# Kernel optimization log

Hardware: AMD Instinct MI355X
Metric: run time of the kernel (lower is better)

## Reference

```python
import jax, jax.numpy as jnp
import numpy as np

B, T, E, H, V = 128, 400, 128, 128, 50000
H2, H4, H6 = 2 * H, 4 * H, 6 * H


def setup_inputs() -> dict:
    key = jax.random.key(0)
    ks = jax.random.split(key, 16)
    s = 0.05
    return dict(
        input_ids=jax.random.randint(ks[0], (B, 1), 0, V),
        pre_hidden=jax.random.normal(ks[1], (1, B, H2), jnp.float32),
        pre_cell=jax.random.normal(ks[2], (1, B, H2), jnp.float32),
        enc_outputs=jax.random.normal(ks[3], (B, T, H2), jnp.float32),
        source_input=jax.random.randint(ks[4], (B, T), 0, V),
        coverage=jax.random.uniform(ks[5], (B, 1, T), jnp.float32),
        emb_table=s * jax.random.normal(ks[6], (V, E), jnp.float32),
        w_ih=s * jax.random.normal(ks[7], (4 * H2, E), jnp.float32),
        w_hh=s * jax.random.normal(ks[8], (4 * H2, H2), jnp.float32),
        b_ih=jnp.zeros((4 * H2,), jnp.float32),
        b_hh=jnp.zeros((4 * H2,), jnp.float32),
        w_align=s * jax.random.normal(ks[9], (1, H6), jnp.float32),
        b_align=jnp.zeros((1,), jnp.float32),
        w_cov=s * jax.random.normal(ks[10], (H2, 1), jnp.float32),
        b_cov=jnp.zeros((H2,), jnp.float32),
        w_fc1=s * jax.random.normal(ks[11], (H4, H4), jnp.float32),
        b_fc1=jnp.zeros((H4,), jnp.float32),
        w_fc2=s * jax.random.normal(ks[12], (V, H4), jnp.float32),
        b_fc2=jnp.zeros((V,), jnp.float32),
        w_gen=s * jax.random.normal(ks[13], (1, H4 + E), jnp.float32),
        b_gen=jnp.zeros((1,), jnp.float32),
    )


def reference(input_ids, pre_hidden, pre_cell, enc_outputs, source_input, coverage,
              emb_table, w_ih, w_hh, b_ih, b_hh, w_align, b_align, w_cov, b_cov,
              w_fc1, b_fc1, w_fc2, b_fc2, w_gen, b_gen):
    # embedding lookup (flag=False path: no dropout)
    emb = emb_table[input_ids[:, 0]]                      # [B,E]
    # single-step LSTM (PyTorch gate order i,f,g,o; hidden size 2H)
    h0, c0 = pre_hidden[0], pre_cell[0]                   # [B,2H]
    gates = emb @ w_ih.T + b_ih + h0 @ w_hh.T + b_hh      # [B,8H]
    i, f, g, o = jnp.split(gates, 4, axis=-1)
    c = jax.nn.sigmoid(f) * c0 + jax.nn.sigmoid(i) * jnp.tanh(g)
    h = jax.nn.sigmoid(o) * jnp.tanh(c)                   # [B,2H]
    # coverage feature + attention over encoder steps
    cov_feat = coverage.transpose(0, 2, 1) @ w_cov.T + b_cov        # [B,T,2H]
    h_rep = jnp.broadcast_to(h[:, None, :], enc_outputs.shape)     # [B,T,2H]
    combine = jnp.concatenate([enc_outputs, h_rep, cov_feat], -1)  # [B,T,6H]
    scores = jnp.tanh(combine @ w_align.T + b_align)               # [B,T,1]
    attn = jax.nn.softmax(scores, axis=1)                          # [B,T,1]
    attn_bt = attn[:, :, 0]                                        # [B,T]
    cov_bt = coverage[:, 0, :]
    cov_loss = jnp.sum(jnp.minimum(attn_bt, cov_bt))
    new_cov = coverage + attn_bt[:, None, :]                       # [B,1,T]
    # context + vocab distribution
    context = jnp.einsum('bt,bte->be', attn_bt, enc_outputs)       # [B,2H]
    fc = jnp.tanh(jnp.concatenate([h, context], -1) @ w_fc1.T + b_fc1)
    pvocab = jax.nn.softmax(fc @ w_fc2.T + b_fc2, axis=1)          # [B,V]
    # copy distribution: fused batched scatter-add (replaces per-batch one-hot matmul loop)
    b_idx = jnp.arange(attn_bt.shape[0])[:, None]
    copy = jnp.zeros_like(pvocab).at[b_idx, source_input].add(attn_bt)
    # generation probability and mixture
    gen_in = jnp.concatenate([context, h, emb], -1)                # [B,4H+E]
    pgen = jax.nn.sigmoid(gen_in @ w_gen.T + b_gen)                # [B,1]
    out = pvocab * pgen + copy * (1.0 - pgen)
    return (out, h[None], c[None], attn_bt[:, None, :], copy, new_cov, cov_loss)
```

## Files before the change

### kernel.cpp

```cpp
#include <hip/hip_runtime.h>
#include <hip/hip_bf16.h>
#include <math.h>

#define B_  128
#define T_  400
#define E_  128
#define H2_ 256
#define H4_ 512
#define V_  50000
#define G4_ 1024
#define KACT 384

#define OFF_H       6400000
#define OFF_C       6432768
#define OFF_ATTN    6465536
#define OFF_COPY    6516736
#define OFF_NEWCOV 12916736
#define OFF_COVLOSS 12967936

#define WS_ACT   0
#define WS_GATES (WS_ACT + KACT*B_)
#define WS_HC    (WS_GATES + G4_*B_)
#define WS_FCB   (WS_HC + H4_*B_)
#define WS_SC    (WS_FCB + H4_*B_/2)
#define WS_ATTN  (WS_SC + B_*T_)
#define WS_CTXP  (WS_ATTN + B_*T_)
#define WS_SMP   (WS_CTXP + B_*8*H2_)
#define WS_HDOT  (WS_SMP + B_*8*2)
#define WS_COVP  (WS_HDOT + B_)
#define WS_PGEN  (WS_COVP + B_)
#define WS_MAX   (WS_PGEN + B_)
#define WS_INV   (WS_MAX + B_)
#define WS_AB    (WS_INV + B_)

typedef __attribute__((ext_vector_type(8))) short bf16x8;
typedef __attribute__((ext_vector_type(4))) float f32x4;
typedef __attribute__((ext_vector_type(16))) float f32x16;

__device__ inline float sigmoidf_(float x){ return 1.f/(1.f+__expf(-x)); }

__device__ inline short f2bf(float x){
  __hip_bfloat16 h = __float2bfloat16(x);
  return *reinterpret_cast<short*>(&h);
}

__device__ inline float blk_reduce_sum(float v, float* red){
  int t = threadIdx.x;
  red[t] = v; __syncthreads();
  for (int s = 128; s > 0; s >>= 1){ if (t < s) red[t] += red[t+s]; __syncthreads(); }
  float r = red[0]; __syncthreads(); return r;
}
__device__ inline float blk_reduce_max(float v, float* red){
  int t = threadIdx.x;
  red[t] = v; __syncthreads();
  for (int s = 128; s > 0; s >>= 1){ if (t < s) red[t] = fmaxf(red[t], red[t+s]); __syncthreads(); }
  float r = red[0]; __syncthreads(); return r;
}

__global__ __launch_bounds__(256) void k_zero(float* __restrict__ p){
  size_t i = ((size_t)blockIdx.x*256 + threadIdx.x)*4;
  if (i < (size_t)B_*V_)
    *(float4*)&p[i] = make_float4(0.f,0.f,0.f,0.f);
}

__global__ __launch_bounds__(256) void k_act(const int* __restrict__ ids,
    const float* __restrict__ pre_h, const float* __restrict__ emb_table,
    const float* __restrict__ w_align, const float* __restrict__ w_cov,
    const float* __restrict__ b_cov, float* __restrict__ act,
    float* __restrict__ ab){
  __shared__ float red[256];
  int t = threadIdx.x;
  int idx = blockIdx.x*256 + t;
  int k = idx >> 7, b = idx & 127;
  float v = (k < E_) ? emb_table[(size_t)ids[b]*E_ + k]
                     : pre_h[b*H2_ + (k - E_)];
  act[idx] = v;
  if (blockIdx.x == 0) {
    float wa = w_align[2*H2_ + t];
    float alpha = blk_reduce_sum(w_cov[t]*wa, red);
    float beta  = blk_reduce_sum(b_cov[t]*wa, red);
    if (t == 0) { ab[0] = alpha; ab[1] = beta; }
  }
}

__global__ __launch_bounds__(256) void k_gates(const float* __restrict__ act,
    const float* __restrict__ w_ih, const float* __restrict__ w_hh,
    const float* __restrict__ b_ih, const float* __restrict__ b_hh,
    float* __restrict__ gates){
  __shared__ float wt[8][KACT];
  int t = threadIdx.x; int j0 = blockIdx.x*8;
  for (int idx = t; idx < 8*KACT; idx += 256) {
    int r = idx / KACT, k = idx % KACT;
    int j = j0 + r;
    wt[r][k] = (k < E_) ? w_ih[j*E_ + k] : w_hh[j*H2_ + (k - E_)];
  }
  __syncthreads();
  int jq = t >> 7, b = t & 127;
  float acc[4] = {0.f,0.f,0.f,0.f};
  for (int k = 0; k < KACT; ++k) {
    float a = act[k*B_ + b];
    #pragma unroll
    for (int jj = 0; jj < 4; ++jj) acc[jj] += wt[jq*4+jj][k]*a;
  }
  #pragma unroll
  for (int jj = 0; jj < 4; ++jj) {
    int j = j0 + jq*4 + jj;
    gates[j*B_ + b] = acc[jj] + b_ih[j] + b_hh[j];
  }
}

__global__ __launch_bounds__(256) void k_lstm(const float* __restrict__ gates,
    const float* __restrict__ pre_c, const float* __restrict__ w_align,
    float* __restrict__ o_h, float* __restrict__ o_c,
    float* __restrict__ hc, float* __restrict__ hdot){
  __shared__ float red[256];
  int b = blockIdx.x, k = threadIdx.x;
  float i_ = gates[(0*H2_ + k)*B_ + b];
  float f_ = gates[(1*H2_ + k)*B_ + b];
  float g_ = gates[(2*H2_ + k)*B_ + b];
  float o_ = gates[(3*H2_ + k)*B_ + b];
  float c = sigmoidf_(f_)*pre_c[b*H2_ + k] + sigmoidf_(i_)*tanhf(g_);
  float h = sigmoidf_(o_)*tanhf(c);
  o_h[b*H2_ + k] = h;
  o_c[b*H2_ + k] = c;
  hc[k*B_ + b] = h;
  float s = blk_reduce_sum(h * w_align[H2_ + k], red);
  if (k == 0) hdot[b] = s;
}

__global__ __launch_bounds__(256) void k_scores(const float* __restrict__ enc,
    const float* __restrict__ cov, const float* __restrict__ w_align,
    const float* __restrict__ b_align, const float* __restrict__ hdot,
    const float* __restrict__ ab, float* __restrict__ sc){
  int b = blockIdx.y, c = blockIdx.x;
  int t = threadIdx.x, wave = t >> 6, lane = t & 63;
  float4 wa4 = *(const float4*)&w_align[lane*4];
  float hd = hdot[b], alpha = ab[0], beta = ab[1], ba = b_align[0];
  int t0 = c*50;
  for (int tt = t0 + wave; tt < t0 + 50; tt += 4) {
    const float4* ep = (const float4*)&enc[((size_t)b*T_ + tt)*H2_];
    float4 e4 = ep[lane];
    float d = e4.x*wa4.x + e4.y*wa4.y + e4.z*wa4.z + e4.w*wa4.w;
    #pragma unroll
    for (int m = 32; m >= 1; m >>= 1) d += __shfl_xor(d, m);
    if (lane == 0)
      sc[b*T_ + tt] = tanhf(d + hd + alpha*cov[b*T_ + tt] + beta + ba);
  }
}

__global__ __launch_bounds__(256) void k_soft(const float* __restrict__ sc_in,
    const float* __restrict__ cov, const int* __restrict__ src,
    float* __restrict__ o_attn, float* __restrict__ o_newcov,
    float* __restrict__ o_copy, float* __restrict__ covp,
    float* __restrict__ attn_ws){
  __shared__ float red[256];
  int b = blockIdx.x, t = threadIdx.x;
  float x1 = sc_in[b*T_ + t];
  float x2 = (t + 256 < T_) ? sc_in[b*T_ + t + 256] : -1e30f;
  float mx = blk_reduce_max(fmaxf(x1, x2), red);
  float e1 = __expf(x1 - mx);
  float e2 = (t + 256 < T_) ? __expf(x2 - mx) : 0.f;
  float sum = blk_reduce_sum(e1 + e2, red);
  float inv = 1.f/sum;
  float cl;
  {
    float a1 = e1*inv; float c1 = cov[b*T_ + t];
    attn_ws[b*T_ + t] = a1;
    o_attn[b*T_ + t] = a1;
    o_newcov[b*T_ + t] = c1 + a1;
    atomicAdd(&o_copy[(size_t)b*V_ + src[b*T_ + t]], a1);
    cl = fminf(a1, c1);
  }
  if (t + 256 < T_) {
    float a2 = e2*inv; float c2 = cov[b*T_ + t + 256];
    attn_ws[b*T_ + t + 256] = a2;
    o_attn[b*T_ + t + 256] = a2;
    o_newcov[b*T_ + t + 256] = c2 + a2;
    atomicAdd(&o_copy[(size_t)b*V_ + src[b*T_ + t + 256]], a2);
    cl += fminf(a2, c2);
  }
  float clsum = blk_reduce_sum(cl, red);
  if (t == 0) covp[b] = clsum;
}

__global__ __launch_bounds__(256) void k_ctx(const float* __restrict__ enc,
    const float* __restrict__ attn_ws, float* __restrict__ ctxp){
  __shared__ float a_s[50];
  int b = blockIdx.y, c = blockIdx.x, e = threadIdx.x;
  int t0 = c*50;
  if (e < 50) a_s[e] = attn_ws[b*T_ + t0 + e];
  __syncthreads();
  float acc = 0.f;
  #pragma unroll 5
  for (int i = 0; i < 50; ++i)
    acc += a_s[i] * enc[((size_t)b*T_ + t0 + i)*H2_ + e];
  ctxp[((size_t)b*8 + c)*H2_ + e] = acc;
}

__global__ __launch_bounds__(256) void k_ctxpgen(const float* __restrict__ ctxp,
    const int* __restrict__ ids, const float* __restrict__ emb_table,
    const float* __restrict__ w_gen, const float* __restrict__ b_gen,
    float* __restrict__ hc, float* __restrict__ pgen){
  __shared__ float red[256];
  int b = blockIdx.x, t = threadIdx.x;
  float ctx = 0.f;
  #pragma unroll
  for (int c = 0; c < 8; ++c) ctx += ctxp[((size_t)b*8 + c)*H2_ + t];
  hc[(H2_ + t)*B_ + b] = ctx;
  float p = ctx*w_gen[t] + hc[t*B_ + b]*w_gen[H2_ + t];
  if (t < E_) p += emb_table[(size_t)ids[b]*E_ + t]*w_gen[2*H2_ + t];
  float s = blk_reduce_sum(p, red);
  if (t == 0) pgen[b] = sigmoidf_(s + b_gen[0]);
}

__global__ __launch_bounds__(256) void k_fc1(const float* __restrict__ hc,
    const float* __restrict__ w_fc1, const float* __restrict__ b_fc1,
    short* __restrict__ fcb){
  __shared__ float wt[16][H4_];
  int t = threadIdx.x; int j0 = blockIdx.x*16;
  for (int idx = t; idx < 16*H4_; idx += 256) {
    int r = idx >> 9, k = idx & 511;
    wt[r][k] = w_fc1[(j0 + r)*H4_ + k];
  }
  __syncthreads();
  int jq = t >> 7, b = t & 127;
  float acc[8] = {};
  for (int k = 0; k < H4_; ++k) {
    float a = hc[k*B_ + b];
    #pragma unroll
    for (int jj = 0; jj < 8; ++jj) acc[jj] += wt[jq*8+jj][k]*a;
  }
  bf16x8 pack;
  #pragma unroll
  for (int jj = 0; jj < 8; ++jj) {
    int j = j0 + jq*8 + jj;
    pack[jj] = f2bf(tanhf(acc[jj] + b_fc1[j]));
  }
  *(bf16x8*)&fcb[(size_t)b*H4_ + j0 + jq*8] = pack;
}

__global__ __launch_bounds__(256, 2) void k_gemm2m(const short* __restrict__ fcb,
    const float* __restrict__ w_fc2, const float* __restrict__ b_fc2,
    float* __restrict__ logits){
  __shared__ __attribute__((aligned(16))) char lds[49152];
  int t = threadIdx.x;
  int w = t >> 6, l = t & 63;
  int ln = l & 31, g2 = l >> 5;
  int v0 = blockIdx.x*128;
  int v = v0 + w*32 + ln;
  int vl = w*32 + ln;

  int ar0 = t >> 2,         as0 = t & 3;
  int ar1 = (256 + t) >> 2, as1 = (256 + t) & 3;
  int aoff0 = as0*2048 + ((ar0 ^ (as0 << 1)) & 127)*16;
  int aoff1 = as1*2048 + ((ar1 ^ (as1 << 1)) & 127)*16;
  const short* ag0 = fcb + ar0*H4_ + as0*8;
  const short* ag1 = fcb + ar1*H4_ + as1*8;
  int woffs[4]; const float* wgs[4];
  #pragma unroll
  for (int p = 0; p < 4; ++p) {
    int i = p*256 + t;
    int row = i >> 3, kg = i & 7;
    woffs[p] = 8192 + kg*2048 + ((row ^ kg) & 127)*16;
    int vr = v0 + row; if (vr >= V_) vr = V_ - 1;
    wgs[p] = w_fc2 + (size_t)vr*H4_ + kg*4;
  }

  f32x16 acc0 = {}, acc1 = {}, acc2 = {}, acc3 = {};

  bf16x8 aE0, aE1; f32x4 wE0, wE1, wE2, wE3;
  bf16x8 aO0, aO1; f32x4 wO0, wO1, wO2, wO3;

  #define LOADSET(A0, A1, W0, W1, W2, W3, c) {                                \
    A0 = *(const bf16x8*)(ag0 + (c)*32);                                      \
    A1 = *(const bf16x8*)(ag1 + (c)*32);                                      \
    W0 = *(const f32x4*)(wgs[0] + (c)*32);                                    \
    W1 = *(const f32x4*)(wgs[1] + (c)*32);                                    \
    W2 = *(const f32x4*)(wgs[2] + (c)*32);                                    \
    W3 = *(const f32x4*)(wgs[3] + (c)*32);                                    \
  }
  #define WRITESET(A0, A1, W0, W1, W2, W3, bi) {                              \
    char* bb = lds + (bi)*24576;                                              \
    *(bf16x8*)(bb + aoff0) = A0;                                              \
    *(bf16x8*)(bb + aoff1) = A1;                                              \
    *(f32x4*)(bb + woffs[0]) = W0;                                            \
    *(f32x4*)(bb + woffs[1]) = W1;                                            \
    *(f32x4*)(bb + woffs[2]) = W2;                                            \
    *(f32x4*)(bb + woffs[3]) = W3;                                            \
  }

  LOADSET(aE0, aE1, wE0, wE1, wE2, wE3, 0)
  LOADSET(aO0, aO1, wO0, wO1, wO2, wO3, 1)
  WRITESET(aE0, aE1, wE0, wE1, wE2, wE3, 0)
  LOADSET(aE0, aE1, wE0, wE1, wE2, wE3, 2)
  __syncthreads();

  for (int c = 0; c < 16; ++c) {
    if (c + 1 < 16) {
      if ((c + 1) & 1) {
        WRITESET(aO0, aO1, wO0, wO1, wO2, wO3, 1)
        if (c + 3 < 16) LOADSET(aO0, aO1, wO0, wO1, wO2, wO3, c + 3)
      } else {
        WRITESET(aE0, aE1, wE0, wE1, wE2, wE3, 0)
        if (c + 3 < 16) LOADSET(aE0, aE1, wE0, wE1, wE2, wE3, c + 3)
      }
    }
    char* Ab = lds + (c & 1)*24576;
    char* Wb = Ab + 8192;
    #pragma unroll
    for (int s = 0; s < 2; ++s) {
      int sg = s*2 + g2;
      bf16x8 a0 = *(const bf16x8*)(Ab + sg*2048 + (((0*32+ln) ^ (sg<<1)) & 127)*16);
      bf16x8 a1 = *(const bf16x8*)(Ab + sg*2048 + (((1*32+ln) ^ (sg<<1)) & 127)*16);
      bf16x8 a2 = *(const bf16x8*)(Ab + sg*2048 + (((2*32+ln) ^ (sg<<1)) & 127)*16);
      bf16x8 a3 = *(const bf16x8*)(Ab + sg*2048 + (((3*32+ln) ^ (sg<<1)) & 127)*16);
      int kgA = s*4 + g2*2;
      f32x4 f0 = *(const f32x4*)(Wb + kgA*2048 + ((vl ^ kgA) & 127)*16);
      int kgB = kgA + 1;
      f32x4 f1 = *(const f32x4*)(Wb + kgB*2048 + ((vl ^ kgB) & 127)*16);
      bf16x8 bf;
      bf[0]=f2bf(f0[0]); bf[1]=f2bf(f0[1]); bf[2]=f2bf(f0[2]); bf[3]=f2bf(f0[3]);
      bf[4]=f2bf(f1[0]); bf[5]=f2bf(f1[1]); bf[6]=f2bf(f1[2]); bf[7]=f2bf(f1[3]);
      acc0 = __builtin_amdgcn_mfma_f32_32x32x16_bf16(a0, bf, acc0, 0, 0, 0);
      acc1 = __builtin_amdgcn_mfma_f32_32x32x16_bf16(a1, bf, acc1, 0, 0, 0);
      acc2 = __builtin_amdgcn_mfma_f32_32x32x16_bf16(a2, bf, acc2, 0, 0, 0);
      acc3 = __builtin_amdgcn_mfma_f32_32x32x16_bf16(a3, bf, acc3, 0, 0, 0);
    }
    __syncthreads();
  }
  #undef LOADSET
  #undef WRITESET

  if (v < V_) {
    float bias = b_fc2[v];
    #pragma unroll
    for (int r = 0; r < 16; ++r) {
      int brow = (r & 3) + 8*(r >> 2) + 4*g2;
      logits[(size_t)(brow)*V_ + v]      = acc0[r] + bias;
      logits[(size_t)(32 + brow)*V_ + v] = acc1[r] + bias;
      logits[(size_t)(64 + brow)*V_ + v] = acc2[r] + bias;
      logits[(size_t)(96 + brow)*V_ + v] = acc3[r] + bias;
    }
  }
}

__global__ __launch_bounds__(256) void k_smp(const float* __restrict__ logits,
    float* __restrict__ smp){
  __shared__ float rm[256], rs[256];
  int b = blockIdx.y, c = blockIdx.x, t = threadIdx.x;
  int v0 = c*6250, v1 = v0 + 6250;
  float m = -1e30f, s = 0.f;
  for (int v = v0 + t; v < v1; v += 256) {
    float x = logits[(size_t)b*V_ + v];
    float nm = fmaxf(m, x);
    s = s*__expf(m - nm) + __expf(x - nm);
    m = nm;
  }
  rm[t] = m; rs[t] = s; __syncthreads();
  for (int k = 128; k > 0; k >>= 1) {
    if (t < k) {
      float m1 = rm[t], s1 = rs[t], m2 = rm[t+k], s2 = rs[t+k];
      float nm = fmaxf(m1, m2);
      rm[t] = nm; rs[t] = s1*__expf(m1-nm) + s2*__expf(m2-nm);
    }
    __syncthreads();
  }
  if (t == 0) { smp[(b*8+c)*2] = rm[0]; smp[(b*8+c)*2+1] = rs[0]; }
}

__global__ __launch_bounds__(128) void k_smred_cl(const float* __restrict__ smp,
    const float* __restrict__ covp, float* __restrict__ mx,
    float* __restrict__ inv, float* __restrict__ o_cl){
  __shared__ float red[128];
  int t = threadIdx.x;
  float m = -1e30f, s = 0.f;
  #pragma unroll
  for (int c = 0; c < 8; ++c) {
    float m2 = smp[(t*8+c)*2], s2 = smp[(t*8+c)*2+1];
    float nm = fmaxf(m, m2);
    s = s*__expf(m - nm) + s2*__expf(m2 - nm);
    m = nm;
  }
  mx[t] = m; inv[t] = 1.f/s;
  red[t] = covp[t]; __syncthreads();
  for (int k = 64; k > 0; k >>= 1){ if (t < k) red[t] += red[t+k]; __syncthreads(); }
  if (t == 0) o_cl[0] = red[0];
}

__global__ __launch_bounds__(256) void k_final(const float* __restrict__ copy,
    const float* __restrict__ mx, const float* __restrict__ inv_s,
    const float* __restrict__ pgen, float* __restrict__ out){
  size_t gid = (size_t)blockIdx.x*256 + threadIdx.x;
  int b = (int)(gid / (V_/4));
  int v = (int)(gid % (V_/4))*4;
  size_t idx = (size_t)b*V_ + v;
  float m = mx[b], is = inv_s[b], pg = pgen[b];
  float4 lg = *(const float4*)&out[idx];
  float4 cp = *(const float4*)&copy[idx];
  float4 o;
  o.x = __expf(lg.x - m)*is*pg + cp.x*(1.f - pg);
  o.y = __expf(lg.y - m)*is*pg + cp.y*(1.f - pg);
  o.z = __expf(lg.z - m)*is*pg + cp.z*(1.f - pg);
  o.w = __expf(lg.w - m)*is*pg + cp.w*(1.f - pg);
  *(float4*)&out[idx] = o;
}

extern "C" void kernel_launch(void* const* d_in, const int* in_sizes, int n_in,
                              void* d_out, int out_size, void* d_ws, size_t ws_size,
                              hipStream_t stream) {
  const int*   ids       = (const int*)  d_in[0];
  const float* pre_h     = (const float*)d_in[1];
  const float* pre_c     = (const float*)d_in[2];
  const float* enc       = (const float*)d_in[3];
  const int*   src       = (const int*)  d_in[4];
  const float* cov       = (const float*)d_in[5];
  const float* emb_table = (const float*)d_in[6];
  const float* w_ih      = (const float*)d_in[7];
  const float* w_hh      = (const float*)d_in[8];
  const float* b_ih      = (const float*)d_in[9];
  const float* b_hh      = (const float*)d_in[10];
  const float* w_align   = (const float*)d_in[11];
  const float* b_align   = (const float*)d_in[12];
  const float* w_cov     = (const float*)d_in[13];
  const float* b_cov     = (const float*)d_in[14];
  const float* w_fc1     = (const float*)d_in[15];
  const float* b_fc1     = (const float*)d_in[16];
  const float* w_fc2     = (const float*)d_in[17];
  const float* b_fc2     = (const float*)d_in[18];
  const float* w_gen     = (const float*)d_in[19];
  const float* b_gen     = (const float*)d_in[20];

  float* out = (float*)d_out;
  float* ws  = (float*)d_ws;

  float* o_out    = out;
  float* o_h      = out + OFF_H;
  float* o_c      = out + OFF_C;
  float* o_attn   = out + OFF_ATTN;
  float* o_copy   = out + OFF_COPY;
  float* o_newcov = out + OFF_NEWCOV;
  float* o_cl     = out + OFF_COVLOSS;

  k_zero <<<(B_*V_/4 + 255)/256, 256, 0, stream>>>(o_copy);
  k_act  <<<192, 256, 0, stream>>>(ids, pre_h, emb_table, w_align, w_cov, b_cov,
                                   ws + WS_ACT, ws + WS_AB);
  k_gates<<<128, 256, 0, stream>>>(ws + WS_ACT, w_ih, w_hh, b_ih, b_hh, ws + WS_GATES);
  k_lstm <<<128, 256, 0, stream>>>(ws + WS_GATES, pre_c, w_align, o_h, o_c,
                                   ws + WS_HC, ws + WS_HDOT);
  k_scores<<<dim3(8,128), 256, 0, stream>>>(enc, cov, w_align, b_align,
                                   ws + WS_HDOT, ws + WS_AB, ws + WS_SC);
  k_soft <<<128, 256, 0, stream>>>(ws + WS_SC, cov, src, o_attn, o_newcov, o_copy,
                                   ws + WS_COVP, ws + WS_ATTN);
  k_ctx  <<<dim3(8,128), 256, 0, stream>>>(enc, ws + WS_ATTN, ws + WS_CTXP);
  k_ctxpgen<<<128, 256, 0, stream>>>(ws + WS_CTXP, ids, emb_table, w_gen, b_gen,
                                   ws + WS_HC, ws + WS_PGEN);
  k_fc1  <<<32, 256, 0, stream>>>(ws + WS_HC, w_fc1, b_fc1, (short*)(ws + WS_FCB));
  k_gemm2m<<<(V_ + 127)/128, 256, 0, stream>>>((const short*)(ws + WS_FCB),
                                   w_fc2, b_fc2, o_out);
  k_smp  <<<dim3(8,128), 256, 0, stream>>>(o_out, ws + WS_SMP);
  k_smred_cl<<<1, 128, 0, stream>>>(ws + WS_SMP, ws + WS_COVP,
                                   ws + WS_MAX, ws + WS_INV, o_cl);
  k_final<<<(int)(((size_t)B_*V_/4)/256), 256, 0, stream>>>(
      o_copy, ws + WS_MAX, ws + WS_INV, ws + WS_PGEN, o_out);
}
```

Baseline: 146.3 us.

## Fuse context computation into score kernel with chunk-local softmax rescaling

The score kernel now keeps each 50-row chunk of encoder outputs in shared memory, computes a chunk-local max and exponentials, and accumulates an unnormalized partial context along with the chunk max. The separate context kernel, which re-read all encoder outputs (about 52 MB), is removed. The pgen kernel rescales the partials using the global max and inverse sum that the softmax kernel now saves. This adds 51 KB of LDS per block, which lowers occupancy. Separately, the fc2 GEMM launch bound is raised to 3 blocks per SM.

```diff
diff --git a/kernel.cpp b/kernel.cpp
--- a/kernel.cpp
+++ b/kernel.cpp
@@ -23,15 +23,17 @@
 #define WS_HC    (WS_GATES + G4_*B_)
 #define WS_FCB   (WS_HC + H4_*B_)
 #define WS_SC    (WS_FCB + H4_*B_/2)
-#define WS_ATTN  (WS_SC + B_*T_)
-#define WS_CTXP  (WS_ATTN + B_*T_)
+#define WS_CTXP  (WS_SC + B_*T_)
 #define WS_SMP   (WS_CTXP + B_*8*H2_)
-#define WS_HDOT  (WS_SMP + B_*8*2)
+#define WS_CHM   (WS_SMP + B_*8*2)
+#define WS_HDOT  (WS_CHM + B_*8)
 #define WS_COVP  (WS_HDOT + B_)
 #define WS_PGEN  (WS_COVP + B_)
 #define WS_MAX   (WS_PGEN + B_)
 #define WS_INV   (WS_MAX + B_)
-#define WS_AB    (WS_INV + B_)
+#define WS_AMX   (WS_INV + B_)
+#define WS_AINV  (WS_AMX + B_)
+#define WS_AB    (WS_AINV + B_)
 
 typedef __attribute__((ext_vector_type(8))) short bf16x8;
 typedef __attribute__((ext_vector_type(4))) float f32x4;
@@ -128,10 +130,14 @@
   if (k == 0) hdot[b] = s;
 }
 
-__global__ __launch_bounds__(256) void k_scores(const float* __restrict__ enc,
+__global__ __launch_bounds__(256) void k_attn2(const float* __restrict__ enc,
     const float* __restrict__ cov, const float* __restrict__ w_align,
     const float* __restrict__ b_align, const float* __restrict__ hdot,
-    const float* __restrict__ ab, float* __restrict__ sc){
+    const float* __restrict__ ab, float* __restrict__ sc,
+    float* __restrict__ ctxp, float* __restrict__ chm){
+  __shared__ float erow[50][H2_];
+  __shared__ float scs[50];
+  __shared__ float red[256];
   int b = blockIdx.y, c = blockIdx.x;
   int t = threadIdx.x, wave = t >> 6, lane = t & 63;
   float4 wa4 = *(const float4*)&w_align[lane*4];
@@ -140,19 +146,32 @@
   for (int tt = t0 + wave; tt < t0 + 50; tt += 4) {
     const float4* ep = (const float4*)&enc[((size_t)b*T_ + tt)*H2_];
     float4 e4 = ep[lane];
+    *(float4*)&erow[tt - t0][lane*4] = e4;
     float d = e4.x*wa4.x + e4.y*wa4.y + e4.z*wa4.z + e4.w*wa4.w;
     #pragma unroll
     for (int m = 32; m >= 1; m >>= 1) d += __shfl_xor(d, m);
-    if (lane == 0)
-      sc[b*T_ + tt] = tanhf(d + hd + alpha*cov[b*T_ + tt] + beta + ba);
-  }
+    if (lane == 0) {
+      float s = tanhf(d + hd + alpha*cov[b*T_ + tt] + beta + ba);
+      scs[tt - t0] = s;
+      sc[b*T_ + tt] = s;
+    }
+  }
+  __syncthreads();
+  float mc = blk_reduce_max(t < 50 ? scs[t] : -1e30f, red);
+  if (t < 50) scs[t] = __expf(scs[t] - mc);
+  __syncthreads();
+  float acc = 0.f;
+  #pragma unroll 5
+  for (int i = 0; i < 50; ++i) acc += scs[i]*erow[i][t];
+  ctxp[((size_t)b*8 + c)*H2_ + t] = acc;
+  if (t == 0) chm[b*8 + c] = mc;
 }
 
 __global__ __launch_bounds__(256) void k_soft(const float* __restrict__ sc_in,
     const float* __restrict__ cov, const int* __restrict__ src,
     float* __restrict__ o_attn, float* __restrict__ o_newcov,
     float* __restrict__ o_copy, float* __restrict__ covp,
-    float* __restrict__ attn_ws){
+    float* __restrict__ amx, float* __restrict__ ainv){
   __shared__ float red[256];
   int b = blockIdx.x, t = threadIdx.x;
   float x1 = sc_in[b*T_ + t];
@@ -162,10 +181,10 @@
   float e2 = (t + 256 < T_) ? __expf(x2 - mx) : 0.f;
   float sum = blk_reduce_sum(e1 + e2, red);
   float inv = 1.f/sum;
+  if (t == 0) { amx[b] = mx; ainv[b] = inv; }
   float cl;
   {
     float a1 = e1*inv; float c1 = cov[b*T_ + t];
-    attn_ws[b*T_ + t] = a1;
     o_attn[b*T_ + t] = a1;
     o_newcov[b*T_ + t] = c1 + a1;
     atomicAdd(&o_copy[(size_t)b*V_ + src[b*T_ + t]], a1);
@@ -173,7 +192,6 @@
   }
   if (t + 256 < T_) {
     float a2 = e2*inv; float c2 = cov[b*T_ + t + 256];
-    attn_ws[b*T_ + t + 256] = a2;
     o_attn[b*T_ + t + 256] = a2;
     o_newcov[b*T_ + t + 256] = c2 + a2;
     atomicAdd(&o_copy[(size_t)b*V_ + src[b*T_ + t + 256]], a2);
@@ -183,29 +201,20 @@
   if (t == 0) covp[b] = clsum;
 }
 
-__global__ __launch_bounds__(256) void k_ctx(const float* __restrict__ enc,
-    const float* __restrict__ attn_ws, float* __restrict__ ctxp){
-  __shared__ float a_s[50];
-  int b = blockIdx.y, c = blockIdx.x, e = threadIdx.x;
-  int t0 = c*50;
-  if (e < 50) a_s[e] = attn_ws[b*T_ + t0 + e];
-  __syncthreads();
-  float acc = 0.f;
-  #pragma unroll 5
-  for (int i = 0; i < 50; ++i)
-    acc += a_s[i] * enc[((size_t)b*T_ + t0 + i)*H2_ + e];
-  ctxp[((size_t)b*8 + c)*H2_ + e] = acc;
-}
-
 __global__ __launch_bounds__(256) void k_ctxpgen(const float* __restrict__ ctxp,
+    const float* __restrict__ chm, const float* __restrict__ amx,
+    const float* __restrict__ ainv,
     const int* __restrict__ ids, const float* __restrict__ emb_table,
     const float* __restrict__ w_gen, const float* __restrict__ b_gen,
     float* __restrict__ hc, float* __restrict__ pgen){
   __shared__ float red[256];
   int b = blockIdx.x, t = threadIdx.x;
+  float M = amx[b], iS = ainv[b];
   float ctx = 0.f;
   #pragma unroll
-  for (int c = 0; c < 8; ++c) ctx += ctxp[((size_t)b*8 + c)*H2_ + t];
+  for (int c = 0; c < 8; ++c)
+    ctx += ctxp[((size_t)b*8 + c)*H2_ + t] * __expf(chm[b*8 + c] - M);
+  ctx *= iS;
   hc[(H2_ + t)*B_ + b] = ctx;
   float p = ctx*w_gen[t] + hc[t*B_ + b]*w_gen[H2_ + t];
   if (t < E_) p += emb_table[(size_t)ids[b]*E_ + t]*w_gen[2*H2_ + t];
@@ -239,7 +248,7 @@
   *(bf16x8*)&fcb[(size_t)b*H4_ + j0 + jq*8] = pack;
 }
 
-__global__ __launch_bounds__(256, 2) void k_gemm2m(const short* __restrict__ fcb,
+__global__ __launch_bounds__(256, 3) void k_gemm2m(const short* __restrict__ fcb,
     const float* __restrict__ w_fc2, const float* __restrict__ b_fc2,
     float* __restrict__ logits){
   __shared__ __attribute__((aligned(16))) char lds[49152];
@@ -447,12 +456,13 @@
   k_gates<<<128, 256, 0, stream>>>(ws + WS_ACT, w_ih, w_hh, b_ih, b_hh, ws + WS_GATES);
   k_lstm <<<128, 256, 0, stream>>>(ws + WS_GATES, pre_c, w_align, o_h, o_c,
                                    ws + WS_HC, ws + WS_HDOT);
-  k_scores<<<dim3(8,128), 256, 0, stream>>>(enc, cov, w_align, b_align,
-                                   ws + WS_HDOT, ws + WS_AB, ws + WS_SC);
+  k_attn2<<<dim3(8,128), 256, 0, stream>>>(enc, cov, w_align, b_align,
+                                   ws + WS_HDOT, ws + WS_AB, ws + WS_SC,
+                                   ws + WS_CTXP, ws + WS_CHM);
   k_soft <<<128, 256, 0, stream>>>(ws + WS_SC, cov, src, o_attn, o_newcov, o_copy,
-                                   ws + WS_COVP, ws + WS_ATTN);
-  k_ctx  <<<dim3(8,128), 256, 0, stream>>>(enc, ws + WS_ATTN, ws + WS_CTXP);
-  k_ctxpgen<<<128, 256, 0, stream>>>(ws + WS_CTXP, ids, emb_table, w_gen, b_gen,
+                                   ws + WS_COVP, ws + WS_AMX, ws + WS_AINV);
+  k_ctxpgen<<<128, 256, 0, stream>>>(ws + WS_CTXP, ws + WS_CHM, ws + WS_AMX,
+                                   ws + WS_AINV, ids, emb_table, w_gen, b_gen,
                                    ws + WS_HC, ws + WS_PGEN);
   k_fc1  <<<32, 256, 0, stream>>>(ws + WS_HC, w_fc1, b_fc1, (short*)(ws + WS_FCB));
   k_gemm2m<<<(V_ + 127)/128, 256, 0, stream>>>((const short*)(ws + WS_FCB),
```

Result: slower. 150.3 us (+2.7%).

## Store logits as bf16 and replace dense copy read with sparse scatter-add

Applied to the files above, without the earlier changes.

The vocab GEMM now writes its logits as bf16 into workspace instead of fp32 into the output buffer, which halves the bytes written by the GEMM and read by the softmax-partial and final kernels. The final mix kernel no longer reads the dense copy tensor. It writes only the scaled softmax term, and a new kernel atomically adds attn*(1-pgen) at the source-token positions. This cuts a full B×V read from the final pass. Rounding logits to bf16 before the exponent adds precision loss in the output probabilities, and the write pattern of the new bf16 stores may be less coalesced.

```diff
diff --git a/kernel.cpp b/kernel.cpp
--- a/kernel.cpp
+++ b/kernel.cpp
@@ -32,6 +32,7 @@
 #define WS_MAX   (WS_PGEN + B_)
 #define WS_INV   (WS_MAX + B_)
 #define WS_AB    (WS_INV + B_)
+#define WS_LOGB  (WS_AB + 16)
 
 typedef __attribute__((ext_vector_type(8))) short bf16x8;
 typedef __attribute__((ext_vector_type(4))) float f32x4;
@@ -42,6 +43,10 @@
 __device__ inline short f2bf(float x){
   __hip_bfloat16 h = __float2bfloat16(x);
   return *reinterpret_cast<short*>(&h);
+}
+__device__ inline float bf2f(unsigned short u){
+  unsigned int x = ((unsigned int)u) << 16;
+  return *reinterpret_cast<float*>(&x);
 }
 
 __device__ inline float blk_reduce_sum(float v, float* red){
@@ -241,7 +246,7 @@
 
 __global__ __launch_bounds__(256, 2) void k_gemm2m(const short* __restrict__ fcb,
     const float* __restrict__ w_fc2, const float* __restrict__ b_fc2,
-    float* __restrict__ logits){
+    short* __restrict__ logb){
   __shared__ __attribute__((aligned(16))) char lds[49152];
   int t = threadIdx.x;
   int w = t >> 6, l = t & 63;
@@ -336,24 +341,27 @@
     #pragma unroll
     for (int r = 0; r < 16; ++r) {
       int brow = (r & 3) + 8*(r >> 2) + 4*g2;
-      logits[(size_t)(brow)*V_ + v]      = acc0[r] + bias;
-      logits[(size_t)(32 + brow)*V_ + v] = acc1[r] + bias;
-      logits[(size_t)(64 + brow)*V_ + v] = acc2[r] + bias;
-      logits[(size_t)(96 + brow)*V_ + v] = acc3[r] + bias;
+      logb[(size_t)(brow)*V_ + v]      = f2bf(acc0[r] + bias);
+      logb[(size_t)(32 + brow)*V_ + v] = f2bf(acc1[r] + bias);
+      logb[(size_t)(64 + brow)*V_ + v] = f2bf(acc2[r] + bias);
+      logb[(size_t)(96 + brow)*V_ + v] = f2bf(acc3[r] + bias);
     }
   }
 }
 
-__global__ __launch_bounds__(256) void k_smp(const float* __restrict__ logits,
+__global__ __launch_bounds__(256) void k_smp(const unsigned short* __restrict__ logb,
     float* __restrict__ smp){
   __shared__ float rm[256], rs[256];
   int b = blockIdx.y, c = blockIdx.x, t = threadIdx.x;
-  int v0 = c*6250, v1 = v0 + 6250;
+  int u0 = c*3125, u1 = u0 + 3125;
+  const unsigned int* lp = (const unsigned int*)(logb + (size_t)b*V_);
   float m = -1e30f, s = 0.f;
-  for (int v = v0 + t; v < v1; v += 256) {
-    float x = logits[(size_t)b*V_ + v];
-    float nm = fmaxf(m, x);
-    s = s*__expf(m - nm) + __expf(x - nm);
+  for (int u = u0 + t; u < u1; u += 256) {
+    unsigned int pr = lp[u];
+    float xa = bf2f((unsigned short)(pr & 0xffff));
+    float xb = bf2f((unsigned short)(pr >> 16));
+    float nm = fmaxf(m, fmaxf(xa, xb));
+    s = s*__expf(m - nm) + __expf(xa - nm) + __expf(xb - nm);
     m = nm;
   }
   rm[t] = m; rs[t] = s; __syncthreads();
@@ -387,22 +395,27 @@
   if (t == 0) o_cl[0] = red[0];
 }
 
-__global__ __launch_bounds__(256) void k_final(const float* __restrict__ copy,
+__global__ __launch_bounds__(256) void k_final(const unsigned short* __restrict__ logb,
     const float* __restrict__ mx, const float* __restrict__ inv_s,
     const float* __restrict__ pgen, float* __restrict__ out){
   size_t gid = (size_t)blockIdx.x*256 + threadIdx.x;
-  int b = (int)(gid / (V_/4));
-  int v = (int)(gid % (V_/4))*4;
-  size_t idx = (size_t)b*V_ + v;
+  int b = (int)(gid / (V_/2));
+  int u = (int)(gid % (V_/2));
   float m = mx[b], is = inv_s[b], pg = pgen[b];
-  float4 lg = *(const float4*)&out[idx];
-  float4 cp = *(const float4*)&copy[idx];
-  float4 o;
-  o.x = __expf(lg.x - m)*is*pg + cp.x*(1.f - pg);
-  o.y = __expf(lg.y - m)*is*pg + cp.y*(1.f - pg);
-  o.z = __expf(lg.z - m)*is*pg + cp.z*(1.f - pg);
-  o.w = __expf(lg.w - m)*is*pg + cp.w*(1.f - pg);
-  *(float4*)&out[idx] = o;
+  unsigned int pr = ((const unsigned int*)(logb + (size_t)b*V_))[u];
+  float2 o;
+  o.x = __expf(bf2f((unsigned short)(pr & 0xffff)) - m)*is*pg;
+  o.y = __expf(bf2f((unsigned short)(pr >> 16)) - m)*is*pg;
+  *(float2*)&out[(size_t)b*V_ + u*2] = o;
+}
+
+__global__ __launch_bounds__(256) void k_scatter(const int* __restrict__ src,
+    const float* __restrict__ attn, const float* __restrict__ pgen,
+    float* __restrict__ out){
+  int b = blockIdx.x, t = threadIdx.x;
+  float c1 = 1.f - pgen[b];
+  for (int tt = t; tt < T_; tt += 256)
+    atomicAdd(&out[(size_t)b*V_ + src[b*T_ + tt]], attn[b*T_ + tt]*c1);
 }
 
 extern "C" void kernel_launch(void* const* d_in, const int* in_sizes, int n_in,
@@ -440,6 +453,7 @@
   float* o_copy   = out + OFF_COPY;
   float* o_newcov = out + OFF_NEWCOV;
   float* o_cl     = out + OFF_COVLOSS;
+  short* logb     = (short*)(ws + WS_LOGB);
 
   k_zero <<<(B_*V_/4 + 255)/256, 256, 0, stream>>>(o_copy);
   k_act  <<<192, 256, 0, stream>>>(ids, pre_h, emb_table, w_align, w_cov, b_cov,
@@ -456,10 +470,11 @@
                                    ws + WS_HC, ws + WS_PGEN);
   k_fc1  <<<32, 256, 0, stream>>>(ws + WS_HC, w_fc1, b_fc1, (short*)(ws + WS_FCB));
   k_gemm2m<<<(V_ + 127)/128, 256, 0, stream>>>((const short*)(ws + WS_FCB),
-                                   w_fc2, b_fc2, o_out);
-  k_smp  <<<dim3(8,128), 256, 0, stream>>>(o_out, ws + WS_SMP);
+                                   w_fc2, b_fc2, logb);
+  k_smp  <<<dim3(8,128), 256, 0, stream>>>((const unsigned short*)logb, ws + WS_SMP);
   k_smred_cl<<<1, 128, 0, stream>>>(ws + WS_SMP, ws + WS_COVP,
                                    ws + WS_MAX, ws + WS_INV, o_cl);
-  k_final<<<(int)(((size_t)B_*V_/4)/256), 256, 0, stream>>>(
-      o_copy, ws + WS_MAX, ws + WS_INV, ws + WS_PGEN, o_out);
-}
+  k_final<<<(int)(((size_t)B_*V_/2)/256), 256, 0, stream>>>(
+      (const unsigned short*)logb, ws + WS_MAX, ws + WS_INV, ws + WS_PGEN, o_out);
+  k_scatter<<<128, 256, 0, stream>>>(src, o_attn, ws + WS_PGEN, o_out);
+}
```

Result: faster. 143.3 us (-2.1%).
